# Kernel tuning notes

Hardware: AMD Instinct MI355X
Metric: run time of the kernel (lower is better)

## Reference

```python
import jax, jax.numpy as jnp
import numpy as np

B, T, C, K, V = 4, 2048, 1024, 1024, 1024
SQRT_K = float(np.sqrt(K))


def setup_inputs() -> dict:
    key = jax.random.key(0)
    ks = jax.random.split(key, 7)
    s = 0.02
    return {
        "x": jax.random.normal(ks[0], (B, T, C), jnp.float32),
        "Wq": (jax.random.normal(ks[1], (C, K), jnp.float32) * s),
        "bq": jnp.zeros((K,), jnp.float32),
        "Wk": (jax.random.normal(ks[2], (C, K), jnp.float32) * s),
        "bk": jnp.zeros((K,), jnp.float32),
        "Wv": (jax.random.normal(ks[3], (C, V), jnp.float32) * s),
        "bv": jnp.zeros((V,), jnp.float32),
    }


def reference(x, Wq, bq, Wk, bk, Wv, bv):
    # projections: [B,T,C] @ [C,K] -> [B,T,K]
    q = x @ Wq + bq
    k = x @ Wk + bk
    v = x @ Wv + bv
    # logits[b,t,s] = q[b,t,:] . k[b,s,:]
    logits = jnp.einsum("btk,bsk->bts", q, k)
    # original mask: mask[j,i] = 1 if i > j -> strict upper triangle masked to -inf
    seq = logits.shape[1]
    mask = jnp.triu(jnp.ones((seq, seq), bool), k=1)
    logits = jnp.where(mask[None, :, :], -jnp.inf, logits)
    # NOTE: original softmax is over dim=1 (query axis), not the key axis
    probs = jax.nn.softmax(logits / SQRT_K, axis=1)
    read = jnp.einsum("bts,bsv->btv", probs, v)
    return jnp.concatenate((x, read), axis=2)
```

## Files before the change

### kernel.cpp

```cpp
#include <hip/hip_runtime.h>
#include <hip/hip_bf16.h>
#include <stdint.h>

#define DEVI __device__ __forceinline__

using u16 = unsigned short;
typedef __attribute__((ext_vector_type(8))) _Float16 halfx8;
typedef __attribute__((ext_vector_type(8))) unsigned short u16x8;
typedef __attribute__((ext_vector_type(4))) float f32x4;

constexpr int BB = 4, TT = 2048, CC = 1024, KD = 1024, VD = 1024;
constexpr int QKVW = 3072;
constexpr int OUTW = CC + VD;
constexpr float INV_SQRT_K = 0.03125f;

DEVI u16 f2h(float f) {
  _Float16 h = (_Float16)f;
  return __builtin_bit_cast(u16, h);
}
DEVI float h2f(u16 u) {
  return (float)__builtin_bit_cast(_Float16, u);
}

DEVI void gload16(const u16* g, u16* l) {
  __builtin_amdgcn_global_load_lds(
      (const __attribute__((address_space(1))) void*)g,
      (__attribute__((address_space(3))) void*)l, 16, 0, 0);
}

__global__ void cast_x_copy(const float* __restrict__ x, u16* __restrict__ xh,
                            float* __restrict__ out) {
  size_t i = (size_t)blockIdx.x * blockDim.x + threadIdx.x;
  float4 v = reinterpret_cast<const float4*>(x)[i];
  ushort4 u;
  u.x = f2h(v.x); u.y = f2h(v.y); u.z = f2h(v.z); u.w = f2h(v.w);
  reinterpret_cast<ushort4*>(xh)[i] = u;
  size_t e = i * 4;
  size_t bt = e / CC;
  int c = (int)(e % CC);
  *reinterpret_cast<float4*>(&out[bt * OUTW + c]) = v;
}

__global__ void transpose_cast_w3(const float* __restrict__ Wq,
                                  const float* __restrict__ Wk,
                                  const float* __restrict__ Wv,
                                  u16* __restrict__ Wt) {
  __shared__ float tile[32][33];
  const float* W = (blockIdx.z == 0) ? Wq : (blockIdx.z == 1) ? Wk : Wv;
  u16* dst = Wt + (size_t)blockIdx.z * 1024 * 1024;
  int n0 = blockIdx.x * 32, c0 = blockIdx.y * 32;
  int tx = threadIdx.x, ty = threadIdx.y;
  for (int i = ty; i < 32; i += 8)
    tile[i][tx] = W[(size_t)(c0 + i) * KD + n0 + tx];
  __syncthreads();
  for (int i = ty; i < 32; i += 8)
    dst[(size_t)(n0 + i) * CC + c0 + tx] = f2h(tile[tx][i]);
}

__global__ void concat_bias(const float* __restrict__ bq, const float* __restrict__ bk,
                            const float* __restrict__ bv, float* __restrict__ bc) {
  int n = blockIdx.x * 256 + threadIdx.x;
  float v = (n < 1024) ? bq[n] : (n < 2048) ? bk[n - 1024] : bv[n - 2048];
  bc[n] = v;
}

__global__ void transpose_v(const u16* __restrict__ QKV, const float* __restrict__ Dp,
                            u16* __restrict__ Vt) {
  __shared__ u16 tile[32][33];
  int b = blockIdx.z;
  int n0 = blockIdx.x * 32, s0 = blockIdx.y * 32;
  const u16* src = QKV + (size_t)b * TT * QKVW + 2048;
  u16* dst = Vt + (size_t)b * VD * TT;
  int tx = threadIdx.x, ty = threadIdx.y;
  for (int i = ty; i < 32; i += 8)
    tile[i][tx] = src[(size_t)(s0 + i) * QKVW + n0 + tx];
  const int s = s0 + tx;
  float d = 0.f;
  for (int rt = s >> 8; rt < TT / 256; ++rt)
    d += Dp[((size_t)rt * BB + b) * TT + s];
  float di = 1.f / d;
  __syncthreads();
  for (int i = ty; i < 32; i += 8)
    dst[(size_t)(n0 + i) * TT + s0 + tx] = f2h(h2f(tile[tx][i]) * di);
}

template <typename OutT, int SWZ, bool CSKIP, bool KLIM, bool BIAS, bool CMASK>
__global__ __launch_bounds__(512, 2) void gemm_bt(
    const u16* __restrict__ A, const u16* __restrict__ Bm, OutT* __restrict__ Out,
    const float* __restrict__ bias, float* __restrict__ Dp,
    int Kd, int lda, int ldb, int ldo,
    long long strA, long long strB, long long strO, float alpha) {
  constexpr int BM = 256, BN = 128, BK = 32;
  constexpr int WM = 4, WN = 2;
  constexpr int WR = 64, WC = 64;
  constexpr int MR = 4, NR = 4;
  constexpr int ASZ = BM * BK, BSZ = BN * BK;
  __shared__ u16 sA[3 * ASZ];
  __shared__ u16 sB[3 * BSZ];
  __shared__ float reds[CMASK ? WM : 1][CMASK ? BN : 1];

  int bx = blockIdx.x, by = blockIdx.y;
  if constexpr (KLIM) {
    bx = gridDim.x - 1 - bx;
  } else if constexpr (SWZ == 1) {
    const int gx = gridDim.x;
    const int nx = gx >> 3;
    int fid = bx + gx * by;
    int xcd = fid & 7, idx = fid >> 3;
    bx = xcd * nx + idx % nx;
    by = idx / nx;
  }
  const int r0 = bx * BM, c0 = by * BN;
  if (CSKIP && c0 > r0 + BM - 1) return;
  A   += (size_t)blockIdx.z * strA;
  Bm  += (size_t)blockIdx.z * strB;
  Out += (size_t)blockIdx.z * strO;

  const int tid = threadIdx.x;
  const int lane = tid & 63;
  const int w = tid >> 6;
  const int wm = w / WN, wn = w % WN;
  const int l15 = lane & 15, l4 = lane >> 4;
  const int cswz8 = 8 * (l4 ^ ((l15 >> 1) & 3));

  const int srow = tid >> 2;
  const int sc8 = 8 * ((tid & 3) ^ ((tid >> 3) & 3));
  const u16* gA  = A  + (size_t)(r0 + srow) * lda + sc8;
  const u16* gA2 = gA + (size_t)128 * lda;
  const u16* gB  = Bm + (size_t)(c0 + srow) * ldb + sc8;
  const int sdst = tid * 8;

  f32x4 acc[MR][NR] = {};

  int kmax = Kd;
  if (KLIM) { int km = r0 + BM; kmax = km < Kd ? km : Kd; }
  const int NT = kmax / BK;

  auto stage = [&](int buf, int kt) {
    const int k0 = kt * BK;
    u16* da = sA + buf * ASZ + sdst;
    gload16(gA + k0, da);
    gload16(gA2 + k0, da + 4096);
    u16* db = sB + buf * BSZ + sdst;
    gload16(gB + k0, db);
  };

  stage(0, 0);
  stage(1, 1);
  asm volatile("s_waitcnt vmcnt(3)" ::: "memory");
  __builtin_amdgcn_s_barrier();

  int buf = 0;
  for (int kt = 0; kt < NT; ++kt) {
    int nb = buf + 2; if (nb >= 3) nb -= 3;
    const u16* rA = sA + buf * ASZ;
    const u16* rB = sB + buf * BSZ;
    halfx8 af[MR], bfv[NR];
#pragma unroll
    for (int n = 0; n < NR; ++n)
      bfv[n] = *reinterpret_cast<const halfx8*>(&rB[(wn * WC + n * 16 + l15) * BK + cswz8]);
#pragma unroll
    for (int m = 0; m < MR; ++m)
      af[m] = *reinterpret_cast<const halfx8*>(&rA[(wm * WR + m * 16 + l15) * BK + cswz8]);
    if (kt + 2 < NT) stage(nb, kt + 2);
    __builtin_amdgcn_s_setprio(1);
#pragma unroll
    for (int m = 0; m < MR; ++m)
#pragma unroll
      for (int n = 0; n < NR; ++n)
        acc[m][n] = __builtin_amdgcn_mfma_f32_16x16x32_f16(af[m], bfv[n], acc[m][n], 0, 0, 0);
    __builtin_amdgcn_s_setprio(0);
    if (kt + 2 < NT)      asm volatile("s_waitcnt vmcnt(3)" ::: "memory");
    else if (kt + 1 < NT) asm volatile("s_waitcnt vmcnt(0)" ::: "memory");
    if (kt + 1 < NT) __builtin_amdgcn_s_barrier();
    buf = buf + 1; if (buf == 3) buf = 0;
  }

  if constexpr (CMASK) {
#pragma unroll
    for (int n = 0; n < NR; ++n) {
      const int gcol = c0 + wn * WC + n * 16 + l15;
      float sm = 0.f;
#pragma unroll
      for (int m = 0; m < MR; ++m) {
        const int growb = r0 + wm * WR + m * 16 + l4 * 4;
#pragma unroll
        for (int r = 0; r < 4; ++r) {
          float p = 0.f;
          if (growb + r >= gcol) p = __expf(acc[m][n][r] * alpha);
          reinterpret_cast<u16*>(Out)[(size_t)(growb + r) * ldo + gcol] = f2h(p);
          sm += p;
        }
      }
      sm += __shfl_xor(sm, 16);
      sm += __shfl_xor(sm, 32);
      if (l4 == 0) reds[wm][wn * WC + n * 16 + l15] = sm;
    }
    __syncthreads();
    if (tid < BN) {
      float d2 = 0.f;
#pragma unroll
      for (int i = 0; i < WM; ++i) d2 += reds[i][tid];
      Dp[((size_t)(r0 >> 8) * BB + blockIdx.z) * TT + c0 + tid] = d2;
    }
  } else {
#pragma unroll
    for (int m = 0; m < MR; ++m) {
      const int growb = r0 + wm * WR + m * 16 + l4 * 4;
#pragma unroll
      for (int n = 0; n < NR; ++n) {
        const int gcol = c0 + wn * WC + n * 16 + l15;
        float bvv = 0.f;
        if (BIAS) bvv = bias[gcol];
#pragma unroll
        for (int r = 0; r < 4; ++r) {
          float val = acc[m][n][r] * alpha + bvv;
          size_t off = (size_t)(growb + r) * ldo + gcol;
          if constexpr (sizeof(OutT) == 2) {
            reinterpret_cast<u16*>(Out)[off] = f2h(val);
          } else {
            reinterpret_cast<float*>(Out)[off] = val;
          }
        }
      }
    }
  }
}

extern "C" void kernel_launch(void* const* d_in, const int* in_sizes, int n_in,
                              void* d_out, int out_size, void* d_ws, size_t ws_size,
                              hipStream_t stream) {
  const float* x  = (const float*)d_in[0];
  const float* Wq = (const float*)d_in[1];
  const float* bq = (const float*)d_in[2];
  const float* Wk = (const float*)d_in[3];
  const float* bk = (const float*)d_in[4];
  const float* Wv = (const float*)d_in[5];
  const float* bv = (const float*)d_in[6];
  float* out = (float*)d_out;
  char* ws = (char*)d_ws;
  constexpr size_t MB = 1024ull * 1024ull;

  u16* xh   = (u16*)(ws);
  u16* QKV  = (u16*)(ws + 16 * MB);
  u16* Wt   = (u16*)(ws + 64 * MB);
  float* bc = (float*)(ws + 70 * MB);
  u16* SP   = (u16*)(ws + 71 * MB);
  u16* Vt = xh;
  float* Dp = (float*)(ws + 64 * MB);

  cast_x_copy<<<dim3((BB * TT * CC / 4) / 256), dim3(256), 0, stream>>>(x, xh, out);
  dim3 tb(32, 8);
  transpose_cast_w3<<<dim3(KD / 32, CC / 32, 3), tb, 0, stream>>>(Wq, Wk, Wv, Wt);
  concat_bias<<<dim3(QKVW / 256), 256, 0, stream>>>(bq, bk, bv, bc);

  gemm_bt<u16, 1, false, false, true, false><<<dim3(32, QKVW / 128, 1), 512, 0, stream>>>(
      xh, Wt, QKV, bc, nullptr, CC, CC, CC, QKVW, 0, 0, 0, 1.f);

  gemm_bt<u16, 0, true, false, false, true><<<dim3(TT / 256, TT / 128, BB), 512, 0, stream>>>(
      QKV, QKV + 1024, SP, nullptr, Dp, KD, QKVW, QKVW, TT,
      (long long)TT * QKVW, (long long)TT * QKVW, (long long)TT * TT, INV_SQRT_K);

  transpose_v<<<dim3(VD / 32, TT / 32, BB), tb, 0, stream>>>(QKV, Dp, Vt);

  gemm_bt<float, 0, false, true, false, false><<<dim3(TT / 256, VD / 128, BB), 512, 0, stream>>>(
      SP, Vt, out + CC, nullptr, nullptr, TT, TT, TT, OUTW,
      (long long)TT * TT, (long long)VD * TT, (long long)TT * OUTW, 1.f);
}
```

Baseline: 187.2 us.

## Use 256x256 tile GEMM with split-half pipelined LDS staging for QKV projection

Adds a new GEMM kernel with a 256x256 output tile, BK=64, XOR-swizzled LDS layout and a four-phase schedule. The schedule interleaves half-tile global-to-LDS loads for the next K step with MFMA work on the current one, and raises wave priority around the MFMA blocks. It replaces the 256x128 tile kernel for the QKV projection only. The larger tile gives more data reuse per LDS load and fewer blocks (384), at the cost of one block per CU, higher register pressure and a lower wave count.

```diff
diff --git a/kernel.cpp b/kernel.cpp
--- a/kernel.cpp
+++ b/kernel.cpp
@@ -84,6 +84,163 @@
     dst[(size_t)(n0 + i) * TT + s0 + tx] = f2h(h2f(tile[tx][i]) * di);
 }
 
+template <typename OutT, int SWZ, bool BIAS>
+__global__ __launch_bounds__(512, 1) void gemm8h(
+    const u16* __restrict__ A, const u16* __restrict__ Bm, OutT* __restrict__ Out,
+    const float* __restrict__ bias, int Kd, int lda, int ldb, int ldo, float alpha) {
+  __shared__ u16 sA[4][8192];
+  __shared__ u16 sB[4][8192];
+
+  int bx = blockIdx.x, by = blockIdx.y;
+  if constexpr (SWZ == 1) {
+    const int gx = gridDim.x;
+    const int nx = gx >> 3;
+    int fid = bx + gx * by;
+    int xcd = fid & 7, idx = fid >> 3;
+    bx = xcd * nx + idx % nx;
+    by = idx / nx;
+  }
+  const int r0 = bx * 256, c0 = by * 256;
+
+  const int tid = threadIdx.x;
+  const int lane = tid & 63;
+  const int w = tid >> 6;
+  const int wm = w >> 2, wn = w & 3;
+  const int l15 = lane & 15, l4 = lane >> 4;
+
+  const int sr = tid >> 3;
+  const int scw = 8 * ((tid & 7) ^ (sr & 7));
+  const u16* gA = A + (size_t)(r0 + sr) * lda + scw;
+  const u16* gB = Bm + (size_t)(c0 + sr) * ldb + scw;
+  const int sdst = tid * 8;
+
+  auto stageA = [&](int db, int h, int kt) {
+    const u16* p = gA + (size_t)h * 128 * lda + kt * 64;
+    u16* d = sA[db * 2 + h] + sdst;
+    gload16(p, d);
+    gload16(p + (size_t)64 * lda, d + 4096);
+  };
+  auto stageB = [&](int db, int h, int kt) {
+    const u16* p = gB + (size_t)h * 128 * ldb + kt * 64;
+    u16* d = sB[db * 2 + h] + sdst;
+    gload16(p, d);
+    gload16(p + (size_t)64 * ldb, d + 4096);
+  };
+  auto rdA = [&](int db, int h, int mm, int ks) {
+    const int row = wm * 64 + mm * 16 + l15;
+    return *reinterpret_cast<const halfx8*>(
+        &sA[db * 2 + h][row * 64 + (((ks * 4 + l4) ^ (l15 & 7)) * 8)]);
+  };
+  auto rdB = [&](int db, int h, int nn, int ks) {
+    const int row = wn * 32 + nn * 16 + l15;
+    return *reinterpret_cast<const halfx8*>(
+        &sB[db * 2 + h][row * 64 + (((ks * 4 + l4) ^ (l15 & 7)) * 8)]);
+  };
+
+  f32x4 acc[8][4] = {};
+  const int NT = Kd / 64;
+
+  stageA(0, 0, 0);
+  stageB(0, 0, 0);
+  stageB(0, 1, 0);
+  stageA(0, 1, 0);
+
+  halfx8 af[4][2], bf01[2][2], bf23[2][2];
+  for (int t = 0; t < NT; ++t) {
+    const int db = t & 1, sdb = db ^ 1;
+    const bool pre = (t + 1 < NT);
+    asm volatile("s_waitcnt vmcnt(4)" ::: "memory");
+    __builtin_amdgcn_s_barrier();
+#pragma unroll
+    for (int mm = 0; mm < 4; ++mm) {
+      af[mm][0] = rdA(db, 0, mm, 0);
+      af[mm][1] = rdA(db, 0, mm, 1);
+    }
+#pragma unroll
+    for (int nn = 0; nn < 2; ++nn) {
+      bf01[nn][0] = rdB(db, 0, nn, 0);
+      bf01[nn][1] = rdB(db, 0, nn, 1);
+    }
+    if (pre) stageA(sdb, 0, t + 1);
+    __builtin_amdgcn_s_setprio(1);
+#pragma unroll
+    for (int mm = 0; mm < 4; ++mm)
+#pragma unroll
+      for (int nn = 0; nn < 2; ++nn)
+#pragma unroll
+        for (int ks = 0; ks < 2; ++ks)
+          acc[mm][nn] = __builtin_amdgcn_mfma_f32_16x16x32_f16(af[mm][ks], bf01[nn][ks], acc[mm][nn], 0, 0, 0);
+    __builtin_amdgcn_s_setprio(0);
+    if (pre) asm volatile("s_waitcnt vmcnt(4)" ::: "memory");
+    else     asm volatile("s_waitcnt vmcnt(2)" ::: "memory");
+    __builtin_amdgcn_s_barrier();
+#pragma unroll
+    for (int nn = 0; nn < 2; ++nn) {
+      bf23[nn][0] = rdB(db, 1, nn, 0);
+      bf23[nn][1] = rdB(db, 1, nn, 1);
+    }
+    if (pre) stageB(sdb, 0, t + 1);
+    __builtin_amdgcn_s_setprio(1);
+#pragma unroll
+    for (int mm = 0; mm < 4; ++mm)
+#pragma unroll
+      for (int nn = 0; nn < 2; ++nn)
+#pragma unroll
+        for (int ks = 0; ks < 2; ++ks)
+          acc[mm][2 + nn] = __builtin_amdgcn_mfma_f32_16x16x32_f16(af[mm][ks], bf23[nn][ks], acc[mm][2 + nn], 0, 0, 0);
+    __builtin_amdgcn_s_setprio(0);
+    if (pre) asm volatile("s_waitcnt vmcnt(4)" ::: "memory");
+    else     asm volatile("s_waitcnt vmcnt(0)" ::: "memory");
+    __builtin_amdgcn_s_barrier();
+#pragma unroll
+    for (int mm = 0; mm < 4; ++mm) {
+      af[mm][0] = rdA(db, 1, mm, 0);
+      af[mm][1] = rdA(db, 1, mm, 1);
+    }
+    if (pre) stageB(sdb, 1, t + 1);
+    __builtin_amdgcn_s_setprio(1);
+#pragma unroll
+    for (int mm = 0; mm < 4; ++mm)
+#pragma unroll
+      for (int nn = 0; nn < 2; ++nn)
+#pragma unroll
+        for (int ks = 0; ks < 2; ++ks)
+          acc[4 + mm][2 + nn] = __builtin_amdgcn_mfma_f32_16x16x32_f16(af[mm][ks], bf23[nn][ks], acc[4 + mm][2 + nn], 0, 0, 0);
+    __builtin_amdgcn_s_setprio(0);
+    if (pre) stageA(sdb, 1, t + 1);
+    __builtin_amdgcn_s_setprio(1);
+#pragma unroll
+    for (int mm = 0; mm < 4; ++mm)
+#pragma unroll
+      for (int nn = 0; nn < 2; ++nn)
+#pragma unroll
+        for (int ks = 0; ks < 2; ++ks)
+          acc[4 + mm][nn] = __builtin_amdgcn_mfma_f32_16x16x32_f16(af[mm][ks], bf01[nn][ks], acc[4 + mm][nn], 0, 0, 0);
+    __builtin_amdgcn_s_setprio(0);
+  }
+
+#pragma unroll
+  for (int m = 0; m < 8; ++m) {
+    const int growb = r0 + (m >> 2) * 128 + wm * 64 + (m & 3) * 16 + l4 * 4;
+#pragma unroll
+    for (int n = 0; n < 4; ++n) {
+      const int gcol = c0 + (n >> 1) * 128 + wn * 32 + (n & 1) * 16 + l15;
+      float bvv = 0.f;
+      if (BIAS) bvv = bias[gcol];
+#pragma unroll
+      for (int r = 0; r < 4; ++r) {
+        float val = acc[m][n][r] * alpha + bvv;
+        size_t off = (size_t)(growb + r) * ldo + gcol;
+        if constexpr (sizeof(OutT) == 2) {
+          reinterpret_cast<u16*>(Out)[off] = f2h(val);
+        } else {
+          reinterpret_cast<float*>(Out)[off] = val;
+        }
+      }
+    }
+  }
+}
+
 template <typename OutT, int SWZ, bool CSKIP, bool KLIM, bool BIAS, bool CMASK>
 __global__ __launch_bounds__(512, 2) void gemm_bt(
     const u16* __restrict__ A, const u16* __restrict__ Bm, OutT* __restrict__ Out,
@@ -254,8 +411,8 @@
   transpose_cast_w3<<<dim3(KD / 32, CC / 32, 3), tb, 0, stream>>>(Wq, Wk, Wv, Wt);
   concat_bias<<<dim3(QKVW / 256), 256, 0, stream>>>(bq, bk, bv, bc);
 
-  gemm_bt<u16, 1, false, false, true, false><<<dim3(32, QKVW / 128, 1), 512, 0, stream>>>(
-      xh, Wt, QKV, bc, nullptr, CC, CC, CC, QKVW, 0, 0, 0, 1.f);
+  gemm8h<u16, 1, true><<<dim3(32, QKVW / 256, 1), 512, 0, stream>>>(
+      xh, Wt, QKV, bc, CC, CC, CC, QKVW, 1.f);
 
   gemm_bt<u16, 0, true, false, false, true><<<dim3(TT / 256, TT / 128, BB), 512, 0, stream>>>(
       QKV, QKV + 1024, SP, nullptr, Dp, KD, QKVW, QKVW, TT,
```

Result: no change. 183.9 us (-1.8%).
